# Performance work log

Hardware: AMD Instinct MI355X
Metric: run time of the kernel (lower is better)

The kernel has to match this reference:

```python
import jax, jax.numpy as jnp
import numpy as np

NUM_HEADS = 12

def setup_inputs() -> dict:
    key = jax.random.key(0)
    k1, k2, k3 = jax.random.split(key, 3)
    B, N, C = 8, 1024, 768
    x = jax.random.normal(k1, (B, N, C), dtype=jnp.float32)
    Wqkv = jax.random.normal(k2, (C, 3 * C), dtype=jnp.float32) * (C ** -0.5)
    bqkv = jnp.zeros((3 * C,), dtype=jnp.float32)
    Wproj = jax.random.normal(k3, (C, C), dtype=jnp.float32) * (C ** -0.5)
    bproj = jnp.zeros((C,), dtype=jnp.float32)
    return {"x": x, "Wqkv": Wqkv, "bqkv": bqkv, "Wproj": Wproj, "bproj": bproj}

def reference(x, Wqkv, bqkv, Wproj, bproj):
    B, N, C = x.shape
    H = NUM_HEADS
    D = C // H
    scale = D ** -0.5
    qkv = x @ Wqkv + bqkv                       # [B,N,3C]
    qkv = qkv.reshape(B, N, 3, H, D)
    q, k, v = qkv[:, :, 0], qkv[:, :, 1], qkv[:, :, 2]  # [B,N,H,D]
    attn = jnp.einsum('bnhd,bmhd->bhnm', q, k) * scale  # [B,H,N,N]
    attn = jax.nn.softmax(attn, axis=-1)
    # dropout is identity in eval mode
    out = jnp.einsum('bhnm,bmhd->bnhd', attn, v).reshape(B, N, C)
    out = out @ Wproj + bproj
    return out
```

## Files before the change

kernel.cpp:

```cpp
#include <hip/hip_runtime.h>
#include <hip/hip_bf16.h>
#include <cstdint>
#include <cstddef>

typedef __bf16 bf16;
typedef __bf16 bf16x8 __attribute__((ext_vector_type(8)));
typedef __bf16 bf16x4 __attribute__((ext_vector_type(4)));
typedef __bf16 bf16x2 __attribute__((ext_vector_type(2)));
typedef float f32x4 __attribute__((ext_vector_type(4)));
typedef float f32x16 __attribute__((ext_vector_type(16)));
typedef unsigned int u32;
typedef u32 u32x4 __attribute__((ext_vector_type(4)));

#define LDS_CAST(p) (__attribute__((address_space(3))) void*)(p)
#define GLB_CAST(p) (const __attribute__((address_space(1))) void*)(p)
#define MFMA16(a, b, c) __builtin_amdgcn_mfma_f32_16x16x32_bf16(a, b, c, 0, 0, 0)
#define MFMA32(a, b, c) __builtin_amdgcn_mfma_f32_32x32x16_bf16(a, b, c, 0, 0, 0)

#if __has_builtin(__builtin_amdgcn_exp2f)
#define EXPF(x) __builtin_amdgcn_exp2f(x)
#define QK_SCALE 0.18033688011112042f
#else
#define EXPF(x) __expf(x)
#define QK_SCALE 0.125f
#endif

static constexpr int BATCH = 8;
static constexpr int NSEQ  = 1024;
static constexpr int CDIM  = 768;
static constexpr int NH    = 12;
static constexpr int HD    = 64;
static constexpr int MTOT  = BATCH * NSEQ;
static constexpr int NC3   = 3 * CDIM;

static constexpr float M_FIX = 12.0f;

static constexpr int TQKV  = (NC3 / 32) * (CDIM / 32);
static constexpr int TPROJ = (CDIM / 32) * (CDIM / 32);
static constexpr int TT    = TQKV + TPROJ;
static constexpr int N4    = MTOT * CDIM / 4;
static constexpr int CASTB = (N4 + 255) / 256;

__device__ inline u32 pkbf(float a, float b) {
    bf16x2 t = { (bf16)a, (bf16)b };
    return __builtin_bit_cast(u32, t);
}

__global__ void prep_kernel(const float* __restrict__ x, bf16* __restrict__ xb,
                            const float* __restrict__ Wqkv, bf16* __restrict__ wqkvt,
                            const float* __restrict__ Wproj, bf16* __restrict__ wprojt)
{
    __shared__ float tile[32][33];
    const int bid = blockIdx.x;
    if (bid < TT) {
        const float* src; bf16* dst; int N, n0, k0;
        if (bid < TQKV) { src = Wqkv;  dst = wqkvt;  N = NC3;
                          n0 = (bid % (NC3 / 32)) * 32;  k0 = (bid / (NC3 / 32)) * 32; }
        else { int t = bid - TQKV; src = Wproj; dst = wprojt; N = CDIM;
               n0 = (t % (CDIM / 32)) * 32;  k0 = (t / (CDIM / 32)) * 32; }
        const int K = CDIM;
        const int tx = threadIdx.x & 31, ty = threadIdx.x >> 5;
#pragma unroll
        for (int p = 0; p < 4; p++)
            tile[ty + p * 8][tx] = src[(size_t)(k0 + ty + p * 8) * N + n0 + tx];
        __syncthreads();
#pragma unroll
        for (int p = 0; p < 4; p++)
            dst[(size_t)(n0 + ty + p * 8) * K + k0 + tx] = (bf16)tile[tx][ty + p * 8];
    } else {
        int i = (bid - TT) * 256 + threadIdx.x;
        if (i < N4) {
            float4 v = ((const float4*)x)[i];
            bf16x4 o = { (bf16)v.x, (bf16)v.y, (bf16)v.z, (bf16)v.w };
            ((bf16x4*)xb)[i] = o;
        }
    }
}

template <int MODE, int BM>
__global__ __launch_bounds__(BM * 2, 4) void gemm_kernel(
    const bf16* __restrict__ A, const bf16* __restrict__ Bt,
    const float* __restrict__ bias, float* __restrict__ outf,
    bf16* __restrict__ q, bf16* __restrict__ kk, bf16* __restrict__ v,
    int Ndim, int K)
{
    constexpr int BN = 128;
    __shared__ alignas(16) bf16 sAB[2][(BM + BN) * 32];
    const int tid  = threadIdx.x;
    const int lane = tid & 63;
    const int quad = lane >> 4;
    const int l16  = lane & 15;
    const int wid  = tid >> 6;
    const int wmI  = wid >> 1;
    const int wnI  = wid & 1;

    const int wg = blockIdx.x;
    const int x  = (wg & 7) * (gridDim.x >> 3) + (wg >> 3);
    const int nTn = Ndim >> 7;
    const int tn = x % nTn, tm = x / nTn;
    const int tmB = tm * BM, tnB = tn * BN;

    int aoff[4], boff[4];
    {
        const int xr = ((quad ^ ((l16 >> 1) & 3)) << 3);
#pragma unroll
        for (int i = 0; i < 4; i++) aoff[i] = (wmI * 64 + i * 16 + l16) * 32 + xr;
#pragma unroll
        for (int j = 0; j < 4; j++) boff[j] = BM * 32 + (wnI * 64 + j * 16 + l16) * 32 + xr;
    }

    const int r0 = tid >> 2;
    const int c0 = (tid & 3) ^ ((r0 >> 1) & 3);
    const bf16* gA0 = A  + (size_t)(tmB + r0) * K + c0 * 8;
    const bf16* gA1 = gA0 + (size_t)(BM / 2) * K;
    const bf16* gB0 = Bt + (size_t)(tnB + r0) * K + c0 * 8;
    const bf16* gB1 = gB0 + (size_t)64 * K;
    const int ldsb = (tid & ~63) * 8;

    auto STAGE = [&](int t, int bsel) {
        const int k0 = t << 5;
        bf16* d = &sAB[bsel][0] + ldsb;
        if constexpr (BM == 256) {
            __builtin_amdgcn_global_load_lds(GLB_CAST(gA0 + k0), LDS_CAST(d),        16, 0, 0);
            __builtin_amdgcn_global_load_lds(GLB_CAST(gA1 + k0), LDS_CAST(d + 4096), 16, 0, 0);
            __builtin_amdgcn_global_load_lds(GLB_CAST(gB0 + k0), LDS_CAST(d + 8192), 16, 0, 0);
        } else {
            __builtin_amdgcn_global_load_lds(GLB_CAST(gA0 + k0), LDS_CAST(d),        16, 0, 0);
            __builtin_amdgcn_global_load_lds(GLB_CAST(gA1 + k0), LDS_CAST(d + 2048), 16, 0, 0);
            __builtin_amdgcn_global_load_lds(GLB_CAST(gB0 + k0), LDS_CAST(d + 4096), 16, 0, 0);
            __builtin_amdgcn_global_load_lds(GLB_CAST(gB1 + k0), LDS_CAST(d + 6144), 16, 0, 0);
        }
    };

    const f32x4 fzero = {0.f, 0.f, 0.f, 0.f};
    f32x4 acc[4][4];
#pragma unroll
    for (int i = 0; i < 4; i++)
#pragma unroll
        for (int j = 0; j < 4; j++) acc[i][j] = fzero;

    const int NT = K >> 5;
    STAGE(0, 0);

    int bsel = 0;
    for (int t = 0; t < NT; ++t) {
        asm volatile("s_waitcnt vmcnt(0)" ::: "memory");
        __builtin_amdgcn_sched_barrier(0);
        __builtin_amdgcn_s_barrier();
        if (t + 1 < NT) STAGE(t + 1, bsel ^ 1);

        const bf16* buf = &sAB[bsel][0];
        bf16x8 af[4], bfr[4];
#pragma unroll
        for (int i = 0; i < 4; i++) af[i]  = *(const bf16x8*)(buf + aoff[i]);
#pragma unroll
        for (int j = 0; j < 4; j++) bfr[j] = *(const bf16x8*)(buf + boff[j]);

        __builtin_amdgcn_s_setprio(1);
#pragma unroll
        for (int i = 0; i < 4; i++)
#pragma unroll
            for (int j = 0; j < 4; j++) acc[i][j] = MFMA16(af[i], bfr[j], acc[i][j]);
        __builtin_amdgcn_s_setprio(0);
        bsel ^= 1;
    }

    if (MODE == 0) {
#pragma unroll
        for (int i = 0; i < 4; i++) {
            int row = tmB + wmI * 64 + i * 16 + quad * 4;
#pragma unroll
            for (int j = 0; j < 4; j++) {
                int col = tnB + wnI * 64 + j * 16 + l16;
                float bv = bias[col];
                float* op = outf + (size_t)row * Ndim + col;
#pragma unroll
                for (int r = 0; r < 4; r++) op[(size_t)r * Ndim] = acc[i][j][r] + bv;
            }
        }
    } else {
#pragma unroll
        for (int i = 0; i < 4; i++) {
            int row = tmB + wmI * 64 + i * 16 + quad * 4;
            int b  = row >> 10;
            int ns = row & 1023;
#pragma unroll
            for (int j = 0; j < 4; j++) {
                int col = tnB + wnI * 64 + j * 16 + l16;
                int t3  = col / 768;
                int rem = col - t3 * 768;
                int h = rem >> 6;
                int d = rem & 63;
                float bv = bias[col];
                if (t3 == 0) {
                    bf16* qp = q + ((size_t)(b * NH + h) * NSEQ + ns) * HD + d;
#pragma unroll
                    for (int r = 0; r < 4; r++)
                        qp[(size_t)r * HD] = (bf16)((acc[i][j][r] + bv) * (float)QK_SCALE);
                } else if (t3 == 1) {
                    bf16* kp = kk + ((size_t)(b * NH + h) * NSEQ + ns) * HD + d;
#pragma unroll
                    for (int r = 0; r < 4; r++) kp[(size_t)r * HD] = (bf16)(acc[i][j][r] + bv);
                } else {
                    bf16x4 pv = { (bf16)(acc[i][j][0] + bv), (bf16)(acc[i][j][1] + bv),
                                  (bf16)(acc[i][j][2] + bv), (bf16)(acc[i][j][3] + bv) };
                    *(bf16x4*)(v + ((size_t)(b * NH + h) * HD + d) * NSEQ + ns) = pv;
                }
            }
        }
    }
}

__global__ __launch_bounds__(256) void attn_kernel(
    const bf16* __restrict__ q, const bf16* __restrict__ k,
    const bf16* __restrict__ v, bf16* __restrict__ o)
{
    __shared__ alignas(16) bf16 sKV[3][8192];
    const int tid  = threadIdx.x;
    const int lane = tid & 63;
    const int w    = tid >> 6;
    const int h    = lane >> 5;
    const int l32  = lane & 31;

    const int wg  = blockIdx.x;
    const int xcd = wg & 7;
    const int idx = wg >> 3;
    const int bh  = xcd * 12 + (idx % 12);
    const int qt  = idx / 12;
    const int b = bh / NH, hh = bh - b * NH;

    const bf16* qb = q + ((size_t)bh * NSEQ + qt * 128) * HD;
    const bf16* kb = k + (size_t)bh * NSEQ * HD;
    const bf16* vb = v + (size_t)bh * HD * NSEQ;

#pragma unroll
    for (int i = 0; i < 4; i++) {
        int slot = w * 256 + i * 64 + lane;
        int r = slot >> 3, cs = slot & 7;
        __builtin_amdgcn_global_load_lds(GLB_CAST(qb + r * HD + ((cs ^ (r & 7)) * 8)),
                                         LDS_CAST(&sKV[2][(w * 256 + i * 64) * 8]), 16, 0, 0);
    }
    auto stageKV = [&](int kt, int buf) {
#pragma unroll
        for (int i = 0; i < 2; i++) {
            int slot = w * 128 + i * 64 + lane;
            int r = slot >> 3, cs = slot & 7;
            int cc = (cs ^ (r & 7)) * 8;
            __builtin_amdgcn_global_load_lds(GLB_CAST(kb + (size_t)(kt * 64 + r) * HD + cc),
                                             LDS_CAST(&sKV[buf][(w * 128 + i * 64) * 8]), 16, 0, 0);
            __builtin_amdgcn_global_load_lds(GLB_CAST(vb + (size_t)r * NSEQ + kt * 64 + cc),
                                             LDS_CAST(&sKV[buf][4096 + (w * 128 + i * 64) * 8]), 16, 0, 0);
        }
    };
    stageKV(0, 0);
    stageKV(1, 1);
    asm volatile("s_waitcnt vmcnt(4)" ::: "memory");
    __builtin_amdgcn_sched_barrier(0);
    __builtin_amdgcn_s_barrier();

    bf16x8 qf[4];
    {
        int row = w * 32 + l32, rxq = row & 7;
#pragma unroll
        for (int cd = 0; cd < 4; cd++)
            qf[cd] = *(const bf16x8*)(&sKV[2][(row * 8 + ((2 * cd + h) ^ rxq)) * 8]);
    }
    asm volatile("s_waitcnt lgkmcnt(0)" ::: "memory");
    __builtin_amdgcn_sched_barrier(0);

    bf16x8 onesA;
#pragma unroll
    for (int i = 0; i < 8; i++) onesA[i] = (bf16)1.0f;

    f32x16 accO[2], accL;
#pragma unroll
    for (int dt = 0; dt < 2; dt++)
#pragma unroll
        for (int i = 0; i < 16; i++) accO[dt][i] = 0.f;
#pragma unroll
    for (int i = 0; i < 16; i++) accL[i] = 0.f;

    const int rx = l32 & 7;
    int bufc = 0;

    for (int kt = 0; kt < 16; kt++) {
        if (kt) {
            if (kt < 15) asm volatile("s_waitcnt vmcnt(4)" ::: "memory");
            else         asm volatile("s_waitcnt vmcnt(0)" ::: "memory");
            __builtin_amdgcn_sched_barrier(0);
            __builtin_amdgcn_s_barrier();
            __builtin_amdgcn_sched_barrier(0);
        }
        if (kt + 2 < 16) {
            int b2 = bufc + 2; if (b2 >= 3) b2 -= 3;
            stageKV(kt + 2, b2);
        }
        const bf16* sKc = &sKV[bufc][0];
        const bf16* sVc = &sKV[bufc][4096];

        f32x16 accS[2];
#pragma unroll
        for (int kvt = 0; kvt < 2; kvt++)
#pragma unroll
            for (int i = 0; i < 16; i++) accS[kvt][i] = 0.f;
        __builtin_amdgcn_s_setprio(1);
#pragma unroll
        for (int cd = 0; cd < 4; cd++)
#pragma unroll
            for (int kvt = 0; kvt < 2; kvt++) {
                int row = kvt * 32 + l32;
                bf16x8 kf = *(const bf16x8*)(sKc + (row * 8 + ((2 * cd + h) ^ rx)) * 8);
                accS[kvt] = MFMA32(kf, qf[cd], accS[kvt]);
            }
        __builtin_amdgcn_s_setprio(0);

        u32 pr[2][4][2];
#pragma unroll
        for (int kvt = 0; kvt < 2; kvt++)
#pragma unroll
            for (int g = 0; g < 4; g++) {
                pr[kvt][g][0] = pkbf(EXPF(accS[kvt][4 * g + 0] - M_FIX),
                                     EXPF(accS[kvt][4 * g + 1] - M_FIX));
                pr[kvt][g][1] = pkbf(EXPF(accS[kvt][4 * g + 2] - M_FIX),
                                     EXPF(accS[kvt][4 * g + 3] - M_FIX));
            }

        bf16x8 pf[4];
#pragma unroll
        for (int c = 0; c < 4; c++) {
            int kvt = c >> 1, c1 = c & 1;
            u32 u00 = pr[kvt][2 * c1][0],     u01 = pr[kvt][2 * c1][1];
            u32 u10 = pr[kvt][2 * c1 + 1][0], u11 = pr[kvt][2 * c1 + 1][1];
            u32 y0 = h ? u10 : u00, y1 = h ? u11 : u01;
            u32 z0 = h ? u00 : u10, z1 = h ? u01 : u11;
            u32 w0 = (u32)__shfl_xor((int)z0, 32);
            u32 w1 = (u32)__shfl_xor((int)z1, 32);
            u32x4 fv = { h ? w0 : y0, h ? w1 : y1, h ? y0 : w0, h ? y1 : w1 };
            pf[c] = __builtin_bit_cast(bf16x8, fv);
        }

        __builtin_amdgcn_s_setprio(1);
#pragma unroll
        for (int c = 0; c < 4; c++) {
#pragma unroll
            for (int dt = 0; dt < 2; dt++) {
                int row = dt * 32 + l32;
                bf16x8 vf = *(const bf16x8*)(sVc + (row * 8 + ((2 * c + h) ^ rx)) * 8);
                accO[dt] = MFMA32(vf, pf[c], accO[dt]);
            }
            accL = MFMA32(onesA, pf[c], accL);
        }
        __builtin_amdgcn_s_setprio(0);

        bufc += 1; if (bufc >= 3) bufc -= 3;
    }

    float inv = 1.f / accL[0];
    bf16* ob = o + ((size_t)b * NSEQ + qt * 128 + w * 32 + l32) * CDIM + hh * HD;
#pragma unroll
    for (int dt = 0; dt < 2; dt++)
#pragma unroll
        for (int g = 0; g < 4; g++) {
            bf16x4 t = { (bf16)(accO[dt][4 * g + 0] * inv), (bf16)(accO[dt][4 * g + 1] * inv),
                         (bf16)(accO[dt][4 * g + 2] * inv), (bf16)(accO[dt][4 * g + 3] * inv) };
            *(bf16x4*)(ob + dt * 32 + 8 * g + 4 * h) = t;
        }
}

extern "C" void kernel_launch(void* const* d_in, const int* in_sizes, int n_in,
                              void* d_out, int out_size, void* d_ws, size_t ws_size,
                              hipStream_t stream)
{
    const float* x     = (const float*)d_in[0];
    const float* Wqkv  = (const float*)d_in[1];
    const float* bqkv  = (const float*)d_in[2];
    const float* Wproj = (const float*)d_in[3];
    const float* bproj = (const float*)d_in[4];
    float* out = (float*)d_out;

    char* ws = (char*)d_ws;
    const size_t MC2 = (size_t)MTOT * CDIM * 2;
    bf16* xb     = (bf16*)ws; ws += MC2;
    bf16* wqkvt  = (bf16*)ws; ws += (size_t)NC3 * CDIM * 2;
    bf16* wprojt = (bf16*)ws; ws += (size_t)CDIM * CDIM * 2;
    bf16* qw     = (bf16*)ws; ws += MC2;
    bf16* kw     = (bf16*)ws; ws += MC2;
    bf16* vw     = (bf16*)ws; ws += MC2;
    bf16* ow     = (bf16*)ws; ws += MC2;

    prep_kernel<<<dim3(TT + CASTB), dim3(256), 0, stream>>>(x, xb, Wqkv, wqkvt, Wproj, wprojt);

    gemm_kernel<1, 256><<<dim3((NC3 / 128) * (MTOT / 256)), dim3(512), 0, stream>>>(
        xb, wqkvt, bqkv, nullptr, qw, kw, vw, NC3, CDIM);

    attn_kernel<<<dim3(768), dim3(256), 0, stream>>>(qw, kw, vw, ow);

    gemm_kernel<0, 128><<<dim3((CDIM / 128) * (MTOT / 128)), dim3(256), 0, stream>>>(
        ow, wprojt, bproj, out, nullptr, nullptr, nullptr, CDIM, CDIM);
}
```

Measured before the change: 193.8 us.

## Triple-buffer GEMM LDS pipeline and use 128x128 tiles for QKV GEMM

Moves the GEMM mainloop from double to triple buffering. It prefetches two k-tiles ahead and waits with a partial vmcnt, so global-to-LDS loads overlap more of the MFMA work and the wait sits after compute. The QKV projection also drops its 256x128, 512-thread tile for the same 128x128, 256-thread tile as the output projection, which doubles the grid. LDS use per block goes up with the third buffer, which may lower occupancy, and A-tile reuse in the QKV GEMM goes down.

```diff
diff --git a/kernel.cpp b/kernel.cpp
--- a/kernel.cpp
+++ b/kernel.cpp
@@ -77,15 +77,15 @@
     }
 }
 
-template <int MODE, int BM>
-__global__ __launch_bounds__(BM * 2, 4) void gemm_kernel(
+template <int MODE>
+__global__ __launch_bounds__(256, 4) void gemm_kernel(
     const bf16* __restrict__ A, const bf16* __restrict__ Bt,
     const float* __restrict__ bias, float* __restrict__ outf,
     bf16* __restrict__ q, bf16* __restrict__ kk, bf16* __restrict__ v,
     int Ndim, int K)
 {
-    constexpr int BN = 128;
-    __shared__ alignas(16) bf16 sAB[2][(BM + BN) * 32];
+    constexpr int BM = 128, BN = 128;
+    __shared__ alignas(16) bf16 sAB[3][(BM + BN) * 32];
     const int tid  = threadIdx.x;
     const int lane = tid & 63;
     const int quad = lane >> 4;
@@ -112,7 +112,7 @@
     const int r0 = tid >> 2;
     const int c0 = (tid & 3) ^ ((r0 >> 1) & 3);
     const bf16* gA0 = A  + (size_t)(tmB + r0) * K + c0 * 8;
-    const bf16* gA1 = gA0 + (size_t)(BM / 2) * K;
+    const bf16* gA1 = gA0 + (size_t)64 * K;
     const bf16* gB0 = Bt + (size_t)(tnB + r0) * K + c0 * 8;
     const bf16* gB1 = gB0 + (size_t)64 * K;
     const int ldsb = (tid & ~63) * 8;
@@ -120,16 +120,10 @@
     auto STAGE = [&](int t, int bsel) {
         const int k0 = t << 5;
         bf16* d = &sAB[bsel][0] + ldsb;
-        if constexpr (BM == 256) {
-            __builtin_amdgcn_global_load_lds(GLB_CAST(gA0 + k0), LDS_CAST(d),        16, 0, 0);
-            __builtin_amdgcn_global_load_lds(GLB_CAST(gA1 + k0), LDS_CAST(d + 4096), 16, 0, 0);
-            __builtin_amdgcn_global_load_lds(GLB_CAST(gB0 + k0), LDS_CAST(d + 8192), 16, 0, 0);
-        } else {
-            __builtin_amdgcn_global_load_lds(GLB_CAST(gA0 + k0), LDS_CAST(d),        16, 0, 0);
-            __builtin_amdgcn_global_load_lds(GLB_CAST(gA1 + k0), LDS_CAST(d + 2048), 16, 0, 0);
-            __builtin_amdgcn_global_load_lds(GLB_CAST(gB0 + k0), LDS_CAST(d + 4096), 16, 0, 0);
-            __builtin_amdgcn_global_load_lds(GLB_CAST(gB1 + k0), LDS_CAST(d + 6144), 16, 0, 0);
-        }
+        __builtin_amdgcn_global_load_lds(GLB_CAST(gA0 + k0), LDS_CAST(d),        16, 0, 0);
+        __builtin_amdgcn_global_load_lds(GLB_CAST(gA1 + k0), LDS_CAST(d + 2048), 16, 0, 0);
+        __builtin_amdgcn_global_load_lds(GLB_CAST(gB0 + k0), LDS_CAST(d + 4096), 16, 0, 0);
+        __builtin_amdgcn_global_load_lds(GLB_CAST(gB1 + k0), LDS_CAST(d + 6144), 16, 0, 0);
     };
 
     const f32x4 fzero = {0.f, 0.f, 0.f, 0.f};
@@ -141,15 +135,19 @@
 
     const int NT = K >> 5;
     STAGE(0, 0);
-
-    int bsel = 0;
+    STAGE(1, 1);
+    asm volatile("s_waitcnt vmcnt(4)" ::: "memory");
+    __builtin_amdgcn_sched_barrier(0);
+    __builtin_amdgcn_s_barrier();
+
+    int bufc = 0;
     for (int t = 0; t < NT; ++t) {
-        asm volatile("s_waitcnt vmcnt(0)" ::: "memory");
-        __builtin_amdgcn_sched_barrier(0);
-        __builtin_amdgcn_s_barrier();
-        if (t + 1 < NT) STAGE(t + 1, bsel ^ 1);
-
-        const bf16* buf = &sAB[bsel][0];
+        if (t + 2 < NT) {
+            int b2 = bufc + 2; if (b2 >= 3) b2 -= 3;
+            STAGE(t + 2, b2);
+        }
+
+        const bf16* buf = &sAB[bufc][0];
         bf16x8 af[4], bfr[4];
 #pragma unroll
         for (int i = 0; i < 4; i++) af[i]  = *(const bf16x8*)(buf + aoff[i]);
@@ -162,7 +160,15 @@
 #pragma unroll
             for (int j = 0; j < 4; j++) acc[i][j] = MFMA16(af[i], bfr[j], acc[i][j]);
         __builtin_amdgcn_s_setprio(0);
-        bsel ^= 1;
+
+        if (t < NT - 1) {
+            if (t + 2 < NT) asm volatile("s_waitcnt vmcnt(4)" ::: "memory");
+            else            asm volatile("s_waitcnt vmcnt(0)" ::: "memory");
+            __builtin_amdgcn_sched_barrier(0);
+            __builtin_amdgcn_s_barrier();
+            __builtin_amdgcn_sched_barrier(0);
+        }
+        bufc += 1; if (bufc >= 3) bufc -= 3;
     }
 
     if (MODE == 0) {
@@ -390,11 +396,11 @@
 
     prep_kernel<<<dim3(TT + CASTB), dim3(256), 0, stream>>>(x, xb, Wqkv, wqkvt, Wproj, wprojt);
 
-    gemm_kernel<1, 256><<<dim3((NC3 / 128) * (MTOT / 256)), dim3(512), 0, stream>>>(
+    gemm_kernel<1><<<dim3((NC3 / 128) * (MTOT / 128)), dim3(256), 0, stream>>>(
         xb, wqkvt, bqkv, nullptr, qw, kw, vw, NC3, CDIM);
 
     attn_kernel<<<dim3(768), dim3(256), 0, stream>>>(qw, kw, vw, ow);
 
-    gemm_kernel<0, 128><<<dim3((CDIM / 128) * (MTOT / 128)), dim3(256), 0, stream>>>(
+    gemm_kernel<0><<<dim3((CDIM / 128) * (MTOT / 128)), dim3(256), 0, stream>>>(
         ow, wprojt, bproj, out, nullptr, nullptr, nullptr, CDIM, CDIM);
 }
```

New measurement: 190.5 us. About the same (-1.7%).
